# Performance work log

Measured on AMD Instinct MI355X. Metric: run time of the kernel, lower is better.

The kernel has to match this reference:

```python
import jax, jax.numpy as jnp
import numpy as np

D = 1024      # embedding_dim
H = 16        # n_heads
HD = D // H   # head_dim
EPS = 1e-05


def layernorm(x, scale, bias):
    # torch.var default is unbiased (ddof=1) in the original module
    mean = jnp.mean(x, axis=-1, keepdims=True)
    var = jnp.var(x, axis=-1, keepdims=True, ddof=1)
    return scale * (x - mean) / jnp.sqrt(var + EPS) + bias


def gelu(x):
    return 0.5 * x * (1 + jnp.tanh(0.79788456 * (x + 0.044715 * x ** 3)))


def setup_inputs() -> dict:
    key = jax.random.key(0)
    ks = jax.random.split(key, 12)
    s = 0.02
    return {
        "x": jax.random.normal(ks[0], (2, 2048, D), dtype=jnp.float32),
        "Wq": jax.random.normal(ks[1], (D, D), dtype=jnp.float32) * s,
        "Wk": jax.random.normal(ks[2], (D, D), dtype=jnp.float32) * s,
        "Wv": jax.random.normal(ks[3], (D, D), dtype=jnp.float32) * s,
        "Wo": jax.random.normal(ks[4], (D, D), dtype=jnp.float32) * s,
        "bo": jnp.zeros((D,), dtype=jnp.float32),
        "W1": jax.random.normal(ks[5], (D, 4 * D), dtype=jnp.float32) * s,
        "b1": jnp.zeros((4 * D,), dtype=jnp.float32),
        "W2": jax.random.normal(ks[6], (4 * D, D), dtype=jnp.float32) * s,
        "b2": jnp.zeros((D,), dtype=jnp.float32),
        "ln1_scale": jnp.ones((D,), dtype=jnp.float32),
        "ln1_bias": jnp.zeros((D,), dtype=jnp.float32),
        "ln2_scale": jnp.ones((D,), dtype=jnp.float32),
        "ln2_bias": jnp.zeros((D,), dtype=jnp.float32),
    }


def reference(x, Wq, Wk, Wv, Wo, bo, W1, b1, W2, b2,
              ln1_scale, ln1_bias, ln2_scale, ln2_bias):
    B, S, _ = x.shape
    # --- attention sub-block (pre-LN) ---
    h = layernorm(x, ln1_scale, ln1_bias)
    q = (h @ Wq).reshape(B, S, H, HD).transpose(0, 2, 1, 3)  # [B,H,S,HD]
    k = (h @ Wk).reshape(B, S, H, HD).transpose(0, 2, 1, 3)
    v = (h @ Wv).reshape(B, S, H, HD).transpose(0, 2, 1, 3)
    scores = jnp.einsum("bhqd,bhkd->bhqk", q, k)             # [B,H,S,S]
    causal = jnp.tril(jnp.ones((S, S), dtype=bool))
    scores = jnp.where(causal, scores, -jnp.inf)
    attn = jax.nn.softmax(scores / jnp.sqrt(jnp.float32(HD)), axis=-1)
    ctx = jnp.einsum("bhqk,bhkd->bhqd", attn, v)
    ctx = ctx.transpose(0, 2, 1, 3).reshape(B, S, H * HD)
    x = x + (ctx @ Wo + bo)
    # --- FFN sub-block (pre-LN) ---
    h = layernorm(x, ln2_scale, ln2_bias)
    x = x + (gelu(h @ W1 + b1) @ W2 + b2)
    return x
```

## Files before the change

kernel.cpp:

```cpp
#include <hip/hip_runtime.h>
#include <hip/hip_bf16.h>
#include <cstdint>

#define D_DIM 1024
#define S_DIM 2048
#define B_DIM 2
#define NROWS 4096
#define H_DIM 16
#define LOG2E 1.4426950408889634f
#define QSCALE (0.125f * LOG2E)

typedef __bf16 bf16x8 __attribute__((ext_vector_type(8)));
typedef float f32x4 __attribute__((ext_vector_type(4)));
typedef unsigned short u16x8 __attribute__((ext_vector_type(8)));

#define MFMA16(a, b, c) __builtin_amdgcn_mfma_f32_16x16x32_bf16(a, b, c, 0, 0, 0)
#define WBAR __builtin_amdgcn_s_barrier()
#define SB0 __builtin_amdgcn_sched_barrier(0)
#define LGKM0 { asm volatile("s_waitcnt lgkmcnt(0)" ::: "memory"); SB0; }
#define VMW(n) asm volatile("s_waitcnt vmcnt(" #n ")" ::: "memory")

__device__ __forceinline__ void async_cp16(const void* g, void* lds) {
  __builtin_amdgcn_global_load_lds(
      (const __attribute__((address_space(1))) void*)(uintptr_t)g,
      (__attribute__((address_space(3))) void*)(uint32_t)(uintptr_t)lds, 16, 0, 0);
}

__device__ __forceinline__ unsigned short f2bf(float f) {
  __hip_bfloat16 h = __float2bfloat16(f);
  return __builtin_bit_cast(unsigned short, h);
}

__device__ __forceinline__ float bf2f(unsigned short u) {
  return __builtin_bit_cast(float, (unsigned int)u << 16);
}

__device__ __forceinline__ float gelu_fast(float v) {
  float u = v * v;
  float w = v * fmaf(u, 0.044715f, 1.f);
  float e = exp2f(w * -2.3022161f);
  return v * __builtin_amdgcn_rcpf(1.f + e);
}

struct TcArgs {
  const float* src[6];
  __hip_bfloat16* dst[6];
  int K[6];
  int N[6];
  int start[6];
};

__global__ __launch_bounds__(256) void transpose_cast6_kernel(TcArgs a) {
  __shared__ float tile[32][33];
  int bid = blockIdx.x, mi = 0;
#pragma unroll
  for (int i = 1; i < 6; i++)
    if (bid >= a.start[i]) mi = i;
  const float* W = a.src[mi];
  __hip_bfloat16* Wt = a.dst[mi];
  int K = a.K[mi], N = a.N[mi];
  int rel = bid - a.start[mi];
  int tilesx = N >> 5;
  int shift = (N == 4096) ? 7 : 5;
  int n0 = (rel & (tilesx - 1)) * 32, k0 = (rel >> shift) * 32;
  int tx = threadIdx.x, ty = threadIdx.y;
#pragma unroll
  for (int i = 0; i < 32; i += 8)
    tile[ty + i][tx] = W[(size_t)(k0 + ty + i) * N + n0 + tx];
  __syncthreads();
#pragma unroll
  for (int i = 0; i < 32; i += 8)
    Wt[(size_t)(n0 + ty + i) * K + k0 + tx] = __float2bfloat16(tile[tx][ty + i]);
}

__global__ __launch_bounds__(256) void ln_kernel(
    const float* __restrict__ x, const float* __restrict__ sc,
    const float* __restrict__ bi, __hip_bfloat16* __restrict__ out) {
  int row = blockIdx.x, t = threadIdx.x;
  float4 v = ((const float4*)(x + (size_t)row * D_DIM))[t];
  float s = v.x + v.y + v.z + v.w;
  float ss = v.x * v.x + v.y * v.y + v.z * v.z + v.w * v.w;
#pragma unroll
  for (int off = 32; off > 0; off >>= 1) {
    s += __shfl_xor(s, off);
    ss += __shfl_xor(ss, off);
  }
  __shared__ float red[8];
  int wid = t >> 6;
  if ((t & 63) == 0) { red[wid] = s; red[4 + wid] = ss; }
  __syncthreads();
  s = red[0] + red[1] + red[2] + red[3];
  ss = red[4] + red[5] + red[6] + red[7];
  float mean = s * (1.f / 1024.f);
  float var = (ss - 1024.f * mean * mean) * (1.f / 1023.f);
  float inv = rsqrtf(var + 1e-5f);
  float4 scv = ((const float4*)sc)[t];
  float4 biv = ((const float4*)bi)[t];
  ushort4 o;
  o.x = f2bf(scv.x * (v.x - mean) * inv + biv.x);
  o.y = f2bf(scv.y * (v.y - mean) * inv + biv.y);
  o.z = f2bf(scv.z * (v.z - mean) * inv + biv.z);
  o.w = f2bf(scv.w * (v.w - mean) * inv + biv.w);
  ((ushort4*)(out + (size_t)row * D_DIM))[t] = o;
}

template <int EPI>
__global__ __launch_bounds__(256) void gemm128_kernel(
    const __hip_bfloat16* __restrict__ A, const __hip_bfloat16* __restrict__ Bt,
    void* __restrict__ Cout, const float* __restrict__ bias,
    const float* __restrict__ resid, __hip_bfloat16* __restrict__ qb,
    __hip_bfloat16* __restrict__ kb, unsigned short* __restrict__ vt,
    int strideA, int strideB, int nkt) {
  __shared__ char lds[65536];
  const int t = threadIdx.x;
  const int lane = t & 63, wid = t >> 6;
  const int ql = lane & 15, g = lane >> 4;
  const int wr = wid >> 1, wc = wid & 1;

  const int nbm = gridDim.x, nby = gridDim.y;
  const int lin = blockIdx.y * nbm + blockIdx.x;
  const int q8 = (nbm * nby) >> 3;
  const int u = (lin & 7) * q8 + (lin >> 3);
  const int gi = u >> 5, wi = u & 31;
  const int gpc = nbm >> 2;
  const int gcol = gi / gpc, grow = gi % gpc;
  const int m0 = (grow * 4 + (wi >> 3)) * 128;
  const int n0 = (gcol * 8 + (wi & 7)) * 128;
  const int sw = (ql & 7) << 4;

  const int srow = t >> 3;
  const int sc16 = (((t & 7) ^ (srow & 7)) << 4);
  const __hip_bfloat16* aB = A + (size_t)(m0 + srow) * strideA + (sc16 >> 1);
  const __hip_bfloat16* bB = Bt + (size_t)(n0 + srow) * strideB + (sc16 >> 1);
  const uint32_t ldsT = (uint32_t)(t * 16);

  auto stg4 = [&](int kt, int s) {
#pragma unroll
    for (int p = 0; p < 4; p++)
      async_cp16(aB + (size_t)(p * 32) * strideA + kt * 64,
                 lds + s * 16384 + p * 4096 + ldsT);
#pragma unroll
    for (int p = 0; p < 4; p++)
      async_cp16(bB + (size_t)(p * 32) * strideB + kt * 64,
                 lds + 32768 + s * 16384 + p * 4096 + ldsT);
  };

  bf16x8 aR[4][2], bR[4][2];
  f32x4 acc[4][4] = {};

  auto ldA = [&](int s) {
    const char* base = lds + s * 16384 + (wr * 64 + ql) * 128;
#pragma unroll
    for (int mi = 0; mi < 4; mi++)
#pragma unroll
      for (int kk = 0; kk < 2; kk++)
        aR[mi][kk] = *(const bf16x8*)(base + mi * 2048 + ((kk * 64 + g * 16) ^ sw));
  };
  auto ldB = [&](int s, int nh) {
    const char* base = lds + 32768 + s * 16384 + (wc * 64 + ql) * 128;
#pragma unroll
    for (int ni = 0; ni < 2; ni++)
#pragma unroll
      for (int kk = 0; kk < 2; kk++)
        bR[nh * 2 + ni][kk] =
            *(const bf16x8*)(base + (nh * 2 + ni) * 2048 + ((kk * 64 + g * 16) ^ sw));
  };
  auto mma = [&](int nh) {
    __builtin_amdgcn_s_setprio(1);
#pragma unroll
    for (int mi = 0; mi < 4; mi++)
#pragma unroll
      for (int ni = 0; ni < 2; ni++) {
        f32x4 c = acc[mi][nh * 2 + ni];
        c = MFMA16(aR[mi][0], bR[nh * 2 + ni][0], c);
        c = MFMA16(aR[mi][1], bR[nh * 2 + ni][1], c);
        acc[mi][nh * 2 + ni] = c;
      }
    __builtin_amdgcn_s_setprio(0);
  };

  stg4(0, 0); stg4(1, 1);
  VMW(8); WBAR;

#pragma unroll 1
  for (int kt = 0; kt < nkt - 2; ++kt) {
    const int s = kt & 1;
    ldA(s); ldB(s, 0);
    LGKM0; mma(0);
    ldB(s, 1);
    LGKM0; WBAR; SB0;
    stg4(kt + 2, s);
    mma(1);
    VMW(8); WBAR;
  }
  ldA(0); ldB(0, 0);
  LGKM0; mma(0);
  ldB(0, 1);
  LGKM0; WBAR;
  mma(1);
  VMW(0); WBAR;
  ldA(1); ldB(1, 0);
  LGKM0; mma(0);
  ldB(1, 1);
  LGKM0; mma(1);

#pragma unroll
  for (int mi = 0; mi < 4; mi++) {
    const int row0 = m0 + wr * 64 + mi * 16 + (g << 2);
#pragma unroll
    for (int ni = 0; ni < 4; ni++) {
      const int col = n0 + wc * 64 + ni * 16 + ql;
      const f32x4 c = acc[mi][ni];
      if (EPI == 0) {
        const int seg = col >> 10;
        const int c1k = col & 1023;
        if (seg < 2) {
          __hip_bfloat16* Ob = seg == 0 ? qb : kb;
          const float sc = seg == 0 ? QSCALE : 1.f;
#pragma unroll
          for (int rr = 0; rr < 4; rr++)
            Ob[(size_t)(row0 + rr) * 1024 + c1k] = __float2bfloat16(c[rr] * sc);
        } else {
          const int h = c1k >> 6, dh = c1k & 63;
          const int bb = row0 >> 11, s0 = row0 & 2047;
          ushort4 pk;
          pk.x = f2bf(c[0]); pk.y = f2bf(c[1]); pk.z = f2bf(c[2]); pk.w = f2bf(c[3]);
          *(ushort4*)(vt + (((size_t)(bb * 16 + h) * 64 + dh) << 11) + s0) = pk;
        }
      } else if (EPI == 1) {
        const float bv = bias[col];
#pragma unroll
        for (int rr = 0; rr < 4; rr++)
          ((__hip_bfloat16*)Cout)[(size_t)(row0 + rr) * 4096 + col] =
              __float2bfloat16(gelu_fast(c[rr] + bv));
      } else {
        const float bv = bias[col];
#pragma unroll
        for (int rr = 0; rr < 4; rr++)
          ((float*)Cout)[(size_t)(row0 + rr) * 1024 + col] =
              c[rr] + bv + resid[(size_t)(row0 + rr) * 1024 + col];
      }
    }
  }
}

__global__ __launch_bounds__(256) void attn_kernel(
    const __hip_bfloat16* __restrict__ Q, const __hip_bfloat16* __restrict__ Kb,
    const __hip_bfloat16* __restrict__ Vt, __hip_bfloat16* __restrict__ ctx) {
  __shared__ unsigned short Ks[2][64 * 64];
  __shared__ unsigned short Vs[2][64 * 64];
  __shared__ alignas(16) unsigned short Ps[4][16 * 64];
  const int t = threadIdx.x;
  const int lane = t & 63, wid = t >> 6;
  const int ql = lane & 15, g = lane >> 4;
  const int bid = blockIdx.x;
  const int r4 = bid >> 8, k8 = (bid >> 5) & 7, bh = bid & 31;
  const int qt = (r4 == 0) ? 31 - k8 : (r4 == 1) ? 16 + k8 : (r4 == 2) ? 15 - k8 : k8;
  const int b = bh >> 4, hh = bh & 15;
  const int wq0 = qt * 64 + wid * 16;
  const __hip_bfloat16* qp = Q + (size_t)b * S_DIM * D_DIM + hh * 64;
  const __hip_bfloat16* kp = Kb + (size_t)b * S_DIM * D_DIM + hh * 64;
  const __hip_bfloat16* vp = Vt + (size_t)bh * 64 * S_DIM;
  const int kvend = qt * 64 + 64;
  const int swz = (ql & 7) << 4;
  const f32x4 z4 = {0.f, 0.f, 0.f, 0.f};

  auto stageKV = [&](int buf, int kv0) {
    const int sub = lane >> 3, c = lane & 7;
#pragma unroll
    for (int i = 0; i < 2; i++) {
      const int row = wid * 16 + i * 8 + sub;
      const int cs = (c ^ (row & 7)) * 8;
      async_cp16(kp + (size_t)(kv0 + row) * D_DIM + cs,
                 (char*)&Ks[buf][0] + (wid * 16 + i * 8) * 128);
      async_cp16(vp + (size_t)row * S_DIM + kv0 + cs,
                 (char*)&Vs[buf][0] + (wid * 16 + i * 8) * 128);
    }
  };

  bf16x8 qf[2];
#pragma unroll
  for (int hf = 0; hf < 2; hf++)
    qf[hf] = *(const bf16x8*)(qp + (size_t)(wq0 + ql) * D_DIM + hf * 32 + g * 8);

  float m = -3.0e38f, lsum = 0.f;
  f32x4 acc[4] = {};
  unsigned short* Pw = Ps[wid];

  stageKV(0, 0);
  __syncthreads();
  int cur = 0;
  for (int kv0 = 0; kv0 < kvend; kv0 += 64) {
    if (kv0 + 64 < kvend) stageKV(cur ^ 1, kv0 + 64);

    if (kv0 <= wq0 + 15) {
      const char* Kt = (const char*)&Ks[cur][0];
      f32x4 st[4];
#pragma unroll
      for (int ks = 0; ks < 4; ks++) {
        bf16x8 k0 = *(const bf16x8*)(Kt + (ks * 16 + ql) * 128 + ((g * 16) ^ swz));
        bf16x8 k1 = *(const bf16x8*)(Kt + (ks * 16 + ql) * 128 + (((4 + g) * 16) ^ swz));
        st[ks] = MFMA16(k1, qf[1], MFMA16(k0, qf[0], z4));
      }
      if (kv0 + 63 > wq0) {
#pragma unroll
        for (int ks = 0; ks < 4; ks++)
#pragma unroll
          for (int r = 0; r < 4; r++)
            if (kv0 + ks * 16 + 4 * g + r > wq0 + ql) st[ks][r] = -3.0e38f;
      }
      float tm = -3.0e38f;
#pragma unroll
      for (int ks = 0; ks < 4; ks++)
#pragma unroll
        for (int r = 0; r < 4; r++) tm = fmaxf(tm, st[ks][r]);
      tm = fmaxf(tm, __shfl_xor(tm, 16));
      tm = fmaxf(tm, __shfl_xor(tm, 32));
      if (!__all(tm <= m + 8.f)) {
        const float mn = fmaxf(m, tm);
        const float alpha = exp2f(m - mn);
        lsum *= alpha;
#pragma unroll
        for (int db = 0; db < 4; db++) acc[db] *= alpha;
        m = mn;
      }
      float psum = 0.f;
#pragma unroll
      for (int ks = 0; ks < 4; ks++) {
        float p0 = exp2f(st[ks][0] - m), p1 = exp2f(st[ks][1] - m);
        float p2 = exp2f(st[ks][2] - m), p3 = exp2f(st[ks][3] - m);
        psum += (p0 + p1) + (p2 + p3);
        ushort4 pk;
        pk.x = f2bf(p0); pk.y = f2bf(p1); pk.z = f2bf(p2); pk.w = f2bf(p3);
        *(ushort4*)((char*)Pw + ql * 128 + ((ks * 32 + 8 * g) ^ swz)) = pk;
      }
      psum += __shfl_xor(psum, 16);
      psum += __shfl_xor(psum, 32);
      lsum += psum;

      const char* Vtl = (const char*)&Vs[cur][0];
#pragma unroll
      for (int ksl = 0; ksl < 2; ksl++) {
        bf16x8 pb = *(const bf16x8*)((const char*)Pw + ql * 128 + ((ksl * 64 + 16 * g) ^ swz));
#pragma unroll
        for (int db = 0; db < 4; db++) {
          bf16x8 va = *(const bf16x8*)(Vtl + (db * 16 + ql) * 128 + (((ksl * 4 + g) * 16) ^ swz));
          acc[db] = MFMA16(va, pb, acc[db]);
        }
      }
    }
    __syncthreads();
    cur ^= 1;
  }

  const float inv = 1.f / lsum;
  unsigned short* cp = (unsigned short*)ctx + (size_t)(b * S_DIM + wq0 + ql) * D_DIM + hh * 64;
#pragma unroll
  for (int db = 0; db < 4; db++)
#pragma unroll
    for (int i = 0; i < 2; i++) {
      unsigned int lo = f2bf(acc[db][2 * i] * inv);
      unsigned int hi = f2bf(acc[db][2 * i + 1] * inv);
      *(unsigned int*)(cp + db * 16 + 4 * g + 2 * i) = lo | (hi << 16);
    }
}

extern "C" void kernel_launch(void* const* d_in, const int* in_sizes, int n_in,
                              void* d_out, int out_size, void* d_ws, size_t ws_size,
                              hipStream_t stream) {
  const float* x = (const float*)d_in[0];
  const float* Wq = (const float*)d_in[1];
  const float* Wk = (const float*)d_in[2];
  const float* Wv = (const float*)d_in[3];
  const float* Wo = (const float*)d_in[4];
  const float* bo = (const float*)d_in[5];
  const float* W1 = (const float*)d_in[6];
  const float* b1 = (const float*)d_in[7];
  const float* W2 = (const float*)d_in[8];
  const float* b2 = (const float*)d_in[9];
  const float* ln1s = (const float*)d_in[10];
  const float* ln1b = (const float*)d_in[11];
  const float* ln2s = (const float*)d_in[12];
  const float* ln2b = (const float*)d_in[13];
  float* out = (float*)d_out;

  char* p = (char*)d_ws;
  auto take = [&](size_t n) { char* r = p; p += (n + 255) & ~(size_t)255; return r; };
  __hip_bfloat16* Wqt = (__hip_bfloat16*)take((size_t)1024 * 1024 * 2);
  __hip_bfloat16* Wkt = (__hip_bfloat16*)take((size_t)1024 * 1024 * 2);
  __hip_bfloat16* Wvt = (__hip_bfloat16*)take((size_t)1024 * 1024 * 2);
  __hip_bfloat16* Wot = (__hip_bfloat16*)take((size_t)1024 * 1024 * 2);
  __hip_bfloat16* W1t = (__hip_bfloat16*)take((size_t)4096 * 1024 * 2);
  __hip_bfloat16* W2t = (__hip_bfloat16*)take((size_t)4096 * 1024 * 2);
  __hip_bfloat16* hbuf = (__hip_bfloat16*)take((size_t)NROWS * 1024 * 2);
  __hip_bfloat16* qbuf = (__hip_bfloat16*)take((size_t)NROWS * 1024 * 2);
  __hip_bfloat16* kbuf = (__hip_bfloat16*)take((size_t)NROWS * 1024 * 2);
  __hip_bfloat16* vtbuf = (__hip_bfloat16*)take((size_t)NROWS * 1024 * 2);
  __hip_bfloat16* ctxbuf = (__hip_bfloat16*)take((size_t)NROWS * 1024 * 2);
  float* x1buf = (float*)take((size_t)NROWS * 1024 * 4);
  __hip_bfloat16* h2buf = (__hip_bfloat16*)take((size_t)NROWS * 1024 * 2);
  __hip_bfloat16* gbuf = (__hip_bfloat16*)take((size_t)NROWS * 4096 * 2);

  TcArgs ta;
  ta.src[0] = Wq;  ta.dst[0] = Wqt;  ta.K[0] = 1024; ta.N[0] = 1024; ta.start[0] = 0;
  ta.src[1] = Wk;  ta.dst[1] = Wkt;  ta.K[1] = 1024; ta.N[1] = 1024; ta.start[1] = 1024;
  ta.src[2] = Wv;  ta.dst[2] = Wvt;  ta.K[2] = 1024; ta.N[2] = 1024; ta.start[2] = 2048;
  ta.src[3] = Wo;  ta.dst[3] = Wot;  ta.K[3] = 1024; ta.N[3] = 1024; ta.start[3] = 3072;
  ta.src[4] = W1;  ta.dst[4] = W1t;  ta.K[4] = 1024; ta.N[4] = 4096; ta.start[4] = 4096;
  ta.src[5] = W2;  ta.dst[5] = W2t;  ta.K[5] = 4096; ta.N[5] = 1024; ta.start[5] = 8192;
  transpose_cast6_kernel<<<12288, dim3(32, 8), 0, stream>>>(ta);

  ln_kernel<<<NROWS, 256, 0, stream>>>(x, ln1s, ln1b, hbuf);

  gemm128_kernel<0><<<dim3(32, 24), 256, 0, stream>>>(
      hbuf, Wqt, nullptr, nullptr, nullptr, qbuf, kbuf, (unsigned short*)vtbuf,
      1024, 1024, 16);

  attn_kernel<<<1024, 256, 0, stream>>>(qbuf, kbuf, vtbuf, ctxbuf);

  gemm128_kernel<2><<<dim3(32, 8), 256, 0, stream>>>(
      ctxbuf, Wot, x1buf, bo, x, nullptr, nullptr, nullptr, 1024, 1024, 16);

  ln_kernel<<<NROWS, 256, 0, stream>>>(x1buf, ln2s, ln2b, h2buf);

  gemm128_kernel<1><<<dim3(32, 32), 256, 0, stream>>>(
      h2buf, W1t, gbuf, b1, nullptr, nullptr, nullptr, nullptr, 1024, 1024, 16);

  gemm128_kernel<2><<<dim3(32, 8), 256, 0, stream>>>(
      gbuf, W2t, out, b2, x1buf, nullptr, nullptr, nullptr, 4096, 4096, 64);
}
```

Before: 202.8 us.

## Process 128 query rows per attention block to reuse staged K/V tiles

Each attention block now covers 128 query rows, with each wave handling two 16-row subtiles, instead of 64 rows. Each K/V tile staged in LDS therefore feeds twice as many MFMAs, which halves global K/V traffic and staging overhead per query. The grid drops to 512 blocks, and the tile-to-block mapping is changed to pair tiles from the two ends of the causal range for balance. The cost is more registers per wave (doubled accumulators, scores and Q fragments), twice the P scratch in LDS, and fewer blocks to fill the GPU.

Result: slower. 218.8 us (+7.9%).

```diff
diff --git a/kernel.cpp b/kernel.cpp
--- a/kernel.cpp
+++ b/kernel.cpp
@@ -249,19 +249,21 @@
     const __hip_bfloat16* __restrict__ Vt, __hip_bfloat16* __restrict__ ctx) {
   __shared__ unsigned short Ks[2][64 * 64];
   __shared__ unsigned short Vs[2][64 * 64];
-  __shared__ alignas(16) unsigned short Ps[4][16 * 64];
+  __shared__ alignas(16) unsigned short Ps[4][32 * 64];
   const int t = threadIdx.x;
   const int lane = t & 63, wid = t >> 6;
   const int ql = lane & 15, g = lane >> 4;
   const int bid = blockIdx.x;
-  const int r4 = bid >> 8, k8 = (bid >> 5) & 7, bh = bid & 31;
-  const int qt = (r4 == 0) ? 31 - k8 : (r4 == 1) ? 16 + k8 : (r4 == 2) ? 15 - k8 : k8;
+  const int half = bid >> 8, r = bid & 255;
+  const int bh = r & 31, qtf = r >> 5;
+  const int qt = half == 0 ? qtf * 2 : 15 - qtf * 2;
   const int b = bh >> 4, hh = bh & 15;
-  const int wq0 = qt * 64 + wid * 16;
+  const int q0 = qt * 128;
+  const int wq0 = q0 + wid * 32;
   const __hip_bfloat16* qp = Q + (size_t)b * S_DIM * D_DIM + hh * 64;
   const __hip_bfloat16* kp = Kb + (size_t)b * S_DIM * D_DIM + hh * 64;
   const __hip_bfloat16* vp = Vt + (size_t)bh * 64 * S_DIM;
-  const int kvend = qt * 64 + 64;
+  const int kvend = q0 + 128;
   const int swz = (ql & 7) << 4;
   const f32x4 z4 = {0.f, 0.f, 0.f, 0.f};
 
@@ -278,13 +280,16 @@
     }
   };
 
-  bf16x8 qf[2];
-#pragma unroll
-  for (int hf = 0; hf < 2; hf++)
-    qf[hf] = *(const bf16x8*)(qp + (size_t)(wq0 + ql) * D_DIM + hf * 32 + g * 8);
-
-  float m = -3.0e38f, lsum = 0.f;
-  f32x4 acc[4] = {};
+  bf16x8 qf[2][2];
+#pragma unroll
+  for (int qs = 0; qs < 2; qs++)
+#pragma unroll
+    for (int hf = 0; hf < 2; hf++)
+      qf[qs][hf] =
+          *(const bf16x8*)(qp + (size_t)(wq0 + qs * 16 + ql) * D_DIM + hf * 32 + g * 8);
+
+  float m[2] = {-3.0e38f, -3.0e38f}, lsum[2] = {0.f, 0.f};
+  f32x4 acc[4][2] = {};
   unsigned short* Pw = Ps[wid];
 
   stageKV(0, 0);
@@ -293,59 +298,74 @@
   for (int kv0 = 0; kv0 < kvend; kv0 += 64) {
     if (kv0 + 64 < kvend) stageKV(cur ^ 1, kv0 + 64);
 
-    if (kv0 <= wq0 + 15) {
+    if (kv0 <= wq0 + 31) {
       const char* Kt = (const char*)&Ks[cur][0];
-      f32x4 st[4];
+      f32x4 st[4][2];
 #pragma unroll
       for (int ks = 0; ks < 4; ks++) {
         bf16x8 k0 = *(const bf16x8*)(Kt + (ks * 16 + ql) * 128 + ((g * 16) ^ swz));
         bf16x8 k1 = *(const bf16x8*)(Kt + (ks * 16 + ql) * 128 + (((4 + g) * 16) ^ swz));
-        st[ks] = MFMA16(k1, qf[1], MFMA16(k0, qf[0], z4));
+#pragma unroll
+        for (int qs = 0; qs < 2; qs++)
+          st[ks][qs] = MFMA16(k1, qf[qs][1], MFMA16(k0, qf[qs][0], z4));
       }
       if (kv0 + 63 > wq0) {
 #pragma unroll
         for (int ks = 0; ks < 4; ks++)
 #pragma unroll
-          for (int r = 0; r < 4; r++)
-            if (kv0 + ks * 16 + 4 * g + r > wq0 + ql) st[ks][r] = -3.0e38f;
-      }
-      float tm = -3.0e38f;
-#pragma unroll
-      for (int ks = 0; ks < 4; ks++)
-#pragma unroll
-        for (int r = 0; r < 4; r++) tm = fmaxf(tm, st[ks][r]);
-      tm = fmaxf(tm, __shfl_xor(tm, 16));
-      tm = fmaxf(tm, __shfl_xor(tm, 32));
-      if (!__all(tm <= m + 8.f)) {
-        const float mn = fmaxf(m, tm);
-        const float alpha = exp2f(m - mn);
-        lsum *= alpha;
-#pragma unroll
-        for (int db = 0; db < 4; db++) acc[db] *= alpha;
-        m = mn;
-      }
-      float psum = 0.f;
-#pragma unroll
-      for (int ks = 0; ks < 4; ks++) {
-        float p0 = exp2f(st[ks][0] - m), p1 = exp2f(st[ks][1] - m);
-        float p2 = exp2f(st[ks][2] - m), p3 = exp2f(st[ks][3] - m);
-        psum += (p0 + p1) + (p2 + p3);
-        ushort4 pk;
-        pk.x = f2bf(p0); pk.y = f2bf(p1); pk.z = f2bf(p2); pk.w = f2bf(p3);
-        *(ushort4*)((char*)Pw + ql * 128 + ((ks * 32 + 8 * g) ^ swz)) = pk;
-      }
-      psum += __shfl_xor(psum, 16);
-      psum += __shfl_xor(psum, 32);
-      lsum += psum;
+          for (int qs = 0; qs < 2; qs++)
+#pragma unroll
+            for (int rr = 0; rr < 4; rr++)
+              if (kv0 + ks * 16 + 4 * g + rr > wq0 + qs * 16 + ql)
+                st[ks][qs][rr] = -3.0e38f;
+      }
+#pragma unroll
+      for (int qs = 0; qs < 2; qs++) {
+        float tm = -3.0e38f;
+#pragma unroll
+        for (int ks = 0; ks < 4; ks++)
+#pragma unroll
+          for (int rr = 0; rr < 4; rr++) tm = fmaxf(tm, st[ks][qs][rr]);
+        tm = fmaxf(tm, __shfl_xor(tm, 16));
+        tm = fmaxf(tm, __shfl_xor(tm, 32));
+        if (!__all(tm <= m[qs] + 8.f)) {
+          const float mn = fmaxf(m[qs], tm);
+          const float alpha = exp2f(m[qs] - mn);
+          lsum[qs] *= alpha;
+#pragma unroll
+          for (int db = 0; db < 4; db++) acc[db][qs] *= alpha;
+          m[qs] = mn;
+        }
+        float psum = 0.f;
+#pragma unroll
+        for (int ks = 0; ks < 4; ks++) {
+          float p0 = exp2f(st[ks][qs][0] - m[qs]), p1 = exp2f(st[ks][qs][1] - m[qs]);
+          float p2 = exp2f(st[ks][qs][2] - m[qs]), p3 = exp2f(st[ks][qs][3] - m[qs]);
+          psum += (p0 + p1) + (p2 + p3);
+          ushort4 pk;
+          pk.x = f2bf(p0); pk.y = f2bf(p1); pk.z = f2bf(p2); pk.w = f2bf(p3);
+          *(ushort4*)((char*)Pw + (qs * 16 + ql) * 128 + ((ks * 32 + 8 * g) ^ swz)) = pk;
+        }
+        psum += __shfl_xor(psum, 16);
+        psum += __shfl_xor(psum, 32);
+        lsum[qs] += psum;
+      }
 
       const char* Vtl = (const char*)&Vs[cur][0];
 #pragma unroll
       for (int ksl = 0; ksl < 2; ksl++) {
-        bf16x8 pb = *(const bf16x8*)((const char*)Pw + ql * 128 + ((ksl * 64 + 16 * g) ^ swz));
+        bf16x8 pb[2];
+#pragma unroll
+        for (int qs = 0; qs < 2; qs++)
+          pb[qs] = *(const bf16x8*)((const char*)Pw + (qs * 16 + ql) * 128 +
+                                    ((ksl * 64 + 16 * g) ^ swz));
 #pragma unroll
         for (int db = 0; db < 4; db++) {
-          bf16x8 va = *(const bf16x8*)(Vtl + (db * 16 + ql) * 128 + (((ksl * 4 + g) * 16) ^ swz));
-          acc[db] = MFMA16(va, pb, acc[db]);
+          bf16x8 va = *(const bf16x8*)(Vtl + (db * 16 + ql) * 128 +
+                                       (((ksl * 4 + g) * 16) ^ swz));
+#pragma unroll
+          for (int qs = 0; qs < 2; qs++)
+            acc[db][qs] = MFMA16(va, pb[qs], acc[db][qs]);
         }
       }
     }
@@ -353,16 +373,20 @@
     cur ^= 1;
   }
 
-  const float inv = 1.f / lsum;
-  unsigned short* cp = (unsigned short*)ctx + (size_t)(b * S_DIM + wq0 + ql) * D_DIM + hh * 64;
-#pragma unroll
-  for (int db = 0; db < 4; db++)
-#pragma unroll
-    for (int i = 0; i < 2; i++) {
-      unsigned int lo = f2bf(acc[db][2 * i] * inv);
-      unsigned int hi = f2bf(acc[db][2 * i + 1] * inv);
-      *(unsigned int*)(cp + db * 16 + 4 * g + 2 * i) = lo | (hi << 16);
-    }
+#pragma unroll
+  for (int qs = 0; qs < 2; qs++) {
+    const float inv = 1.f / lsum[qs];
+    unsigned short* cp = (unsigned short*)ctx +
+                         (size_t)(b * S_DIM + wq0 + qs * 16 + ql) * D_DIM + hh * 64;
+#pragma unroll
+    for (int db = 0; db < 4; db++)
+#pragma unroll
+      for (int i = 0; i < 2; i++) {
+        unsigned int lo = f2bf(acc[db][qs][2 * i] * inv);
+        unsigned int hi = f2bf(acc[db][qs][2 * i + 1] * inv);
+        *(unsigned int*)(cp + db * 16 + 4 * g + 2 * i) = lo | (hi << 16);
+      }
+  }
 }
 
 extern "C" void kernel_launch(void* const* d_in, const int* in_sizes, int n_in,
@@ -416,7 +440,7 @@
       hbuf, Wqt, nullptr, nullptr, nullptr, qbuf, kbuf, (unsigned short*)vtbuf,
       1024, 1024, 16);
 
-  attn_kernel<<<1024, 256, 0, stream>>>(qbuf, kbuf, vtbuf, ctxbuf);
+  attn_kernel<<<512, 256, 0, stream>>>(qbuf, kbuf, vtbuf, ctxbuf);
 
   gemm128_kernel<2><<<dim3(32, 8), 256, 0, stream>>>(
       ctxbuf, Wot, x1buf, bo, x, nullptr, nullptr, nullptr, 1024, 1024, 16);
```
